# Kernel optimization log

Measured on AMD Instinct MI355X. Metric: run time of the kernel, lower is better.

Reference implementation:

```python
import jax, jax.numpy as jnp
import numpy as np

B, S, D_MODEL, H = 4, 2048, 1024, 16
HD = D_MODEL // H  # head dim = 64


def setup_inputs() -> dict:
    key = jax.random.key(0)
    k1, k2, k3, k4 = jax.random.split(key, 4)
    x = jax.random.normal(k1, (B, S, D_MODEL), dtype=jnp.float32)
    # weights stored as [d_in, d_out] so projection is x @ W
    scale = 1.0 / np.sqrt(D_MODEL)
    Wq = jax.random.normal(k2, (D_MODEL, D_MODEL), dtype=jnp.float32) * scale
    Wk = jax.random.normal(k3, (D_MODEL, D_MODEL), dtype=jnp.float32) * scale
    Wv = jax.random.normal(k4, (D_MODEL, D_MODEL), dtype=jnp.float32) * scale
    return {"x": x, "Wq": Wq, "Wk": Wk, "Wv": Wv}


def reference(x, Wq, Wk, Wv):
    b, s, d_in = x.shape
    h, hd = H, HD
    # project and split heads -> [b, h, s, hd]
    q = (x @ Wq).reshape(b, s, h, hd).transpose(0, 2, 1, 3)
    k = (x @ Wk).reshape(b, s, h, hd).transpose(0, 2, 1, 3)
    v = (x @ Wv).reshape(b, s, h, hd).transpose(0, 2, 1, 3)
    # raw scores [b, h, s, s]; causal mask (strict upper triangle -> -inf)
    scores = jnp.einsum("bhqd,bhkd->bhqk", q, k)
    causal = jnp.tril(jnp.ones((s, s), dtype=bool))
    scores = jnp.where(causal, scores, -jnp.inf)
    attn = jax.nn.softmax(scores / jnp.sqrt(jnp.float32(hd)), axis=-1)
    ctx = jnp.einsum("bhqk,bhkd->bhqd", attn, v)
    return ctx.transpose(0, 2, 1, 3).reshape(b, s, h * hd)
```

## Files before the change

kernel.cpp:

```cpp
#include <hip/hip_runtime.h>

typedef unsigned short u16;
typedef unsigned int u32;
typedef __bf16 bf16_t;
typedef bf16_t bf16x8 __attribute__((ext_vector_type(8)));
typedef bf16_t bf16x4_t __attribute__((ext_vector_type(4)));
typedef float f32x4 __attribute__((ext_vector_type(4)));

#define S_LEN 2048
#define DM 1024
#define NH 16
#define HDIM 64
#define PSTR 80

__device__ __forceinline__ u16 f2b(float f) {
  u32 u = __builtin_bit_cast(u32, f);
  u32 r = (u + 0x7FFFu + ((u >> 16) & 1u)) >> 16;
  return (u16)r;
}

__device__ __forceinline__ void gload16(const void* g, void* l) {
  __builtin_amdgcn_global_load_lds((const __attribute__((address_space(1))) void*)g,
                                   (__attribute__((address_space(3))) void*)l,
                                   16, 0, 0);
}

__device__ __forceinline__ bf16x8 ld_bf8(const u16* p) {
  return *reinterpret_cast<const bf16x8*>(p);
}

__device__ __forceinline__ void stage_tile(const u16* __restrict__ base, int stride,
                                           u16* __restrict__ dst, int tid) {
#pragma unroll
  for (int i = 0; i < 2; ++i) {
    int ci = i * 256 + tid;
    int row = ci >> 3, col = ci & 7;
    gload16(base + (size_t)row * stride + ((col ^ (row & 7)) << 3), dst + ci * 8);
  }
}

__device__ __forceinline__ bf16x8 ld_swz(const u16* lds, int row, int chunk) {
  return ld_bf8(lds + row * 64 + ((chunk ^ (row & 7)) << 3));
}

__global__ __launch_bounds__(256) void k_cvt(const float* __restrict__ in, u16* __restrict__ out) {
  int i = (blockIdx.x * 256 + threadIdx.x) * 4;
  float4 v = *reinterpret_cast<const float4*>(in + i);
  ushort4 o = make_ushort4(f2b(v.x), f2b(v.y), f2b(v.z), f2b(v.w));
  *reinterpret_cast<ushort4*>(out + i) = o;
}

__global__ __launch_bounds__(256) void k_wt(const float* __restrict__ W, u16* __restrict__ Wt) {
  __shared__ float t[32][33];
  int n0 = blockIdx.x * 32, k0 = blockIdx.y * 32;
  int tx = threadIdx.x & 31, ty = threadIdx.x >> 5;
#pragma unroll
  for (int i = 0; i < 32; i += 8)
    t[ty + i][tx] = W[(size_t)(k0 + ty + i) * DM + n0 + tx];
  __syncthreads();
#pragma unroll
  for (int i = 0; i < 32; i += 8)
    Wt[(size_t)(n0 + ty + i) * DM + k0 + tx] = f2b(t[tx][ty + i]);
}

__global__ __launch_bounds__(256) void k_gemm(const u16* __restrict__ Xb, const u16* __restrict__ Wt_all,
                                              u16* __restrict__ Out_all, float qscale) {
  __shared__ u16 At[128 * 32];
  __shared__ u16 Bt[128 * 32];
  int j = blockIdx.x;
  int sw = (j & 7) * 192 + (j >> 3);
  int bx = sw % 24, by = sw / 24;
  int tid = threadIdx.x;
  int lane = tid & 63, w = tid >> 6;
  int l15 = lane & 15, lg = lane >> 4;
  int wm = w >> 1, wn = w & 1;
  int n0g = bx * 128, m0 = by * 128;
  int which = n0g >> 10;
  int n0 = n0g & 1023;
  float scale = (which == 0) ? qscale : 1.0f;
  u16* Out = Out_all + (size_t)which * (size_t)(4 * NH * S_LEN * HDIM);
  f32x4 acc[4][4] = {};
  for (int kt = 0; kt < DM / 32; ++kt) {
    int kk = kt * 32;
#pragma unroll
    for (int i = 0; i < 2; ++i) {
      int t2 = i * 256 + tid;
      int row = t2 >> 2, c16 = t2 & 3;
      gload16(Xb + (size_t)(m0 + row) * DM + kk + c16 * 8, At + t2 * 8);
      gload16(Wt_all + (size_t)(n0g + row) * DM + kk + c16 * 8, Bt + t2 * 8);
    }
    __syncthreads();
    bf16x8 af[4], bfr[4];
#pragma unroll
    for (int mi = 0; mi < 4; ++mi)
      af[mi] = ld_bf8(At + (wm * 64 + mi * 16 + l15) * 32 + lg * 8);
#pragma unroll
    for (int ni = 0; ni < 4; ++ni)
      bfr[ni] = ld_bf8(Bt + (wn * 64 + ni * 16 + l15) * 32 + lg * 8);
#pragma unroll
    for (int mi = 0; mi < 4; ++mi)
#pragma unroll
      for (int ni = 0; ni < 4; ++ni)
        acc[mi][ni] = __builtin_amdgcn_mfma_f32_16x16x32_bf16(af[mi], bfr[ni], acc[mi][ni], 0, 0, 0);
    __syncthreads();
  }
#pragma unroll
  for (int mi = 0; mi < 4; ++mi) {
#pragma unroll
    for (int ni = 0; ni < 4; ++ni) {
#pragma unroll
      for (int r = 0; r < 4; ++r) {
        int m = m0 + wm * 64 + mi * 16 + lg * 4 + r;
        int n = n0 + wn * 64 + ni * 16 + l15;
        int b = m >> 11, s = m & 2047;
        int h = n >> 6, hd = n & 63;
        Out[(((size_t)(b * NH + h)) * S_LEN + s) * HDIM + hd] = f2b(acc[mi][ni][r] * scale);
      }
    }
  }
}

__global__ __launch_bounds__(256) void k_vt(const u16* __restrict__ V, u16* __restrict__ Vt) {
  __shared__ u16 t[32][33];
  int hd0 = blockIdx.x * 32, s0 = blockIdx.y * 32;
  size_t base = (size_t)blockIdx.z * S_LEN * HDIM;
  int tx = threadIdx.x & 31, ty = threadIdx.x >> 5;
#pragma unroll
  for (int i = 0; i < 32; i += 8)
    t[ty + i][tx] = V[base + (size_t)(s0 + ty + i) * HDIM + hd0 + tx];
  __syncthreads();
#pragma unroll
  for (int i = 0; i < 32; i += 8)
    Vt[base + (size_t)(hd0 + ty + i) * S_LEN + s0 + tx] = t[tx][ty + i];
}

__device__ __forceinline__ void attn_strip(const u16* __restrict__ Qp, const u16* __restrict__ Kp,
                                           const u16* __restrict__ Vp, float* __restrict__ out,
                                           int b, int h, int qbase, int w, int tid, int lane, int nt,
                                           u16 (*Kd)[64 * 64], u16* __restrict__ Vd,
                                           u16* __restrict__ Pw) {
  int l15 = lane & 15, lg = lane >> 4;
  int qrow = qbase + w * 16;
  bf16x8 qf0 = ld_bf8(Qp + (size_t)(qrow + l15) * HDIM + lg * 8);
  bf16x8 qf1 = ld_bf8(Qp + (size_t)(qrow + l15) * HDIM + 32 + lg * 8);
  f32x4 o[4] = {};
  float ls = 0.f;
  int qa = qrow + l15;

  stage_tile(Kp, HDIM, Kd[0], tid);
  asm volatile("s_waitcnt vmcnt(0)" ::: "memory");
  __builtin_amdgcn_sched_barrier(0);
  __builtin_amdgcn_s_barrier();
  __builtin_amdgcn_sched_barrier(0);

  for (int kt = 0; kt < nt; ++kt) {
    int k0 = kt * 64;
    int cur = kt & 1;
    bool pre = (kt + 1 < nt);
    stage_tile(Vp + k0, S_LEN, Vd, tid);
    if (pre) stage_tile(Kp + (size_t)(k0 + 64) * HDIM, HDIM, Kd[cur ^ 1], tid);

    f32x4 sc[4];
    __builtin_amdgcn_s_setprio(1);
#pragma unroll
    for (int kb = 0; kb < 4; ++kb) {
      bf16x8 kf0 = ld_swz(Kd[cur], kb * 16 + l15, lg);
      bf16x8 kf1 = ld_swz(Kd[cur], kb * 16 + l15, 4 + lg);
      f32x4 z = {};
      z = __builtin_amdgcn_mfma_f32_16x16x32_bf16(kf0, qf0, z, 0, 0, 0);
      sc[kb] = __builtin_amdgcn_mfma_f32_16x16x32_bf16(kf1, qf1, sc[kb] = z, 0, 0, 0);
    }
    __builtin_amdgcn_s_setprio(0);

    if (kt == nt - 1) {
#pragma unroll
      for (int kb = 0; kb < 4; ++kb) {
        bf16x4_t pw;
#pragma unroll
        for (int r = 0; r < 4; ++r) {
          int key = k0 + kb * 16 + lg * 4 + r;
          float e = __builtin_amdgcn_exp2f(sc[kb][r]);
          e = (key > qa) ? 0.f : e;
          ls += e;
          pw[r] = (bf16_t)e;
        }
        *reinterpret_cast<bf16x4_t*>(Pw + l15 * PSTR + kb * 16 + lg * 4) = pw;
      }
    } else {
#pragma unroll
      for (int kb = 0; kb < 4; ++kb) {
        bf16x4_t pw;
#pragma unroll
        for (int r = 0; r < 4; ++r) {
          float e = __builtin_amdgcn_exp2f(sc[kb][r]);
          ls += e;
          pw[r] = (bf16_t)e;
        }
        *reinterpret_cast<bf16x4_t*>(Pw + l15 * PSTR + kb * 16 + lg * 4) = pw;
      }
    }
    asm volatile("" ::: "memory");
    bf16x8 pf0 = ld_bf8(Pw + l15 * PSTR + lg * 8);
    bf16x8 pf1 = ld_bf8(Pw + l15 * PSTR + 32 + lg * 8);

    if (pre) asm volatile("s_waitcnt vmcnt(2) lgkmcnt(0)" ::: "memory");
    else     asm volatile("s_waitcnt vmcnt(0) lgkmcnt(0)" ::: "memory");
    __builtin_amdgcn_sched_barrier(0);
    __builtin_amdgcn_s_barrier();
    __builtin_amdgcn_sched_barrier(0);

    __builtin_amdgcn_s_setprio(1);
#pragma unroll
    for (int n = 0; n < 4; ++n) {
      bf16x8 vf0 = ld_swz(Vd, n * 16 + l15, lg);
      bf16x8 vf1 = ld_swz(Vd, n * 16 + l15, 4 + lg);
      o[n] = __builtin_amdgcn_mfma_f32_16x16x32_bf16(pf0, vf0, o[n], 0, 0, 0);
      o[n] = __builtin_amdgcn_mfma_f32_16x16x32_bf16(pf1, vf1, o[n], 0, 0, 0);
    }
    __builtin_amdgcn_s_setprio(0);

    asm volatile("s_waitcnt vmcnt(0) lgkmcnt(0)" ::: "memory");
    __builtin_amdgcn_sched_barrier(0);
    __builtin_amdgcn_s_barrier();
    __builtin_amdgcn_sched_barrier(0);
  }

  ls += __shfl_xor(ls, 16);
  ls += __shfl_xor(ls, 32);
  float l0 = __shfl(ls, lg * 4 + 0);
  float l1 = __shfl(ls, lg * 4 + 1);
  float l2 = __shfl(ls, lg * 4 + 2);
  float l3 = __shfl(ls, lg * 4 + 3);
  float lsr[4] = {l0, l1, l2, l3};
#pragma unroll
  for (int r = 0; r < 4; ++r) {
    float inv = 1.f / lsr[r];
    int row = qrow + lg * 4 + r;
#pragma unroll
    for (int n = 0; n < 4; ++n)
      out[((size_t)b * S_LEN + row) * DM + h * HDIM + n * 16 + l15] = o[n][r] * inv;
  }
}

__global__ __launch_bounds__(256, 4) void k_attn(const u16* __restrict__ Qb, const u16* __restrict__ Kb,
                                                 const u16* __restrict__ Vtb, float* __restrict__ out) {
  __shared__ u16 Kd[2][64 * 64];
  __shared__ u16 Vd[64 * 64];
  __shared__ u16 Plds[4][16 * PSTR];
  int j = blockIdx.x;
  int m = j >> 3;
  int x = m & 15;
  int bh = (j & 7) + 8 * (m >> 4);
  int tid = threadIdx.x, lane = tid & 63, w = tid >> 6;
  int b = bh >> 4, h = bh & 15;
  const u16* Qp = Qb + (size_t)bh * S_LEN * HDIM;
  const u16* Kp = Kb + (size_t)bh * S_LEN * HDIM;
  const u16* Vp = Vtb + (size_t)bh * HDIM * S_LEN;
  u16* Pw = Plds[w];
  attn_strip(Qp, Kp, Vp, out, b, h, x * 64, w, tid, lane, x + 1, Kd, Vd, Pw);
  attn_strip(Qp, Kp, Vp, out, b, h, (31 - x) * 64, w, tid, lane, 32 - x, Kd, Vd, Pw);
}

extern "C" void kernel_launch(void* const* d_in, const int* in_sizes, int n_in,
                              void* d_out, int out_size, void* d_ws, size_t ws_size,
                              hipStream_t stream) {
  const float* x  = (const float*)d_in[0];
  const float* Wq = (const float*)d_in[1];
  const float* Wk = (const float*)d_in[2];
  const float* Wv = (const float*)d_in[3];
  float* out = (float*)d_out;

  u16* ws  = (u16*)d_ws;
  u16* xb  = ws;
  u16* wqt = xb + 8388608;
  u16* wkt = wqt + 1048576;
  u16* wvt = wkt + 1048576;
  u16* Qb  = wvt + 1048576;
  u16* Kb  = Qb + 8388608;
  u16* Vb  = Kb + 8388608;
  u16* Vtb = Vb + 8388608;

  const float qscale = 0.125f * 1.44269504088896f;

  k_cvt<<<8192, 256, 0, stream>>>(x, xb);
  k_wt<<<dim3(32, 32), 256, 0, stream>>>(Wq, wqt);
  k_wt<<<dim3(32, 32), 256, 0, stream>>>(Wk, wkt);
  k_wt<<<dim3(32, 32), 256, 0, stream>>>(Wv, wvt);
  k_gemm<<<1536, 256, 0, stream>>>(xb, wqt, Qb, qscale);
  k_vt<<<dim3(2, 64, 64), 256, 0, stream>>>(Vb, Vtb);
  k_attn<<<1024, 256, 0, stream>>>(Qb, Kb, Vtb, out);
}
```

Before: 150.2 us.

## Restructure QKV GEMM into double-buffered 256x192 tiles with swizzled LDS

The fused QKV projection GEMM moves from 128x128 tiles with single-buffered K=32 steps to 256x192 tiles, 512 threads, and K=64 steps. LDS is double-buffered with XOR-swizzled layout, and next-tile global->LDS loads are interleaved between MFMA phases. This aims to raise arithmetic intensity per loaded byte, cut barrier and sync overhead per FLOP, and avoid LDS bank conflicts. In exchange it uses more LDS (about 112 KB per block) and more registers, and a 192-wide tile can now straddle the Q/K/V boundary, so the output target is chosen per column.

```diff
diff --git a/kernel.cpp b/kernel.cpp
--- a/kernel.cpp
+++ b/kernel.cpp
@@ -29,8 +29,15 @@
   return *reinterpret_cast<const bf16x8*>(p);
 }
 
-__device__ __forceinline__ void stage_tile(const u16* __restrict__ base, int stride,
-                                           u16* __restrict__ dst, int tid) {
+__device__ __forceinline__ void stage_chunk(const u16* __restrict__ g, int stride,
+                                            u16* __restrict__ dst, int tid) {
+  int srow = tid >> 3;
+  int scol = ((tid & 7) ^ (srow & 7)) << 3;
+  gload16(g + (size_t)srow * stride + scol, dst + tid * 8);
+}
+
+__device__ __forceinline__ void stage_tile256(const u16* __restrict__ base, int stride,
+                                              u16* __restrict__ dst, int tid) {
 #pragma unroll
   for (int i = 0; i < 2; ++i) {
     int ci = i * 256 + tid;
@@ -39,7 +46,7 @@
   }
 }
 
-__device__ __forceinline__ bf16x8 ld_swz(const u16* lds, int row, int chunk) {
+__device__ __forceinline__ bf16x8 ld_swz64(const u16* lds, int row, int chunk) {
   return ld_bf8(lds + row * 64 + ((chunk ^ (row & 7)) << 3));
 }
 
@@ -63,61 +70,102 @@
     Wt[(size_t)(n0 + ty + i) * DM + k0 + tx] = f2b(t[tx][ty + i]);
 }
 
-__global__ __launch_bounds__(256) void k_gemm(const u16* __restrict__ Xb, const u16* __restrict__ Wt_all,
-                                              u16* __restrict__ Out_all, float qscale) {
-  __shared__ u16 At[128 * 32];
-  __shared__ u16 Bt[128 * 32];
+__global__ __launch_bounds__(512, 2) void k_gemm(const u16* __restrict__ Xb, const u16* __restrict__ Wt_all,
+                                                 u16* __restrict__ Out_all, float qscale) {
+  __shared__ __attribute__((aligned(16))) u16 Asb[2][256 * 64];
+  __shared__ __attribute__((aligned(16))) u16 Bsb[2][192 * 64];
   int j = blockIdx.x;
-  int sw = (j & 7) * 192 + (j >> 3);
-  int bx = sw % 24, by = sw / 24;
+  int sw = (j & 7) * 64 + (j >> 3);
+  int bx = sw & 15, by = sw >> 4;
+  int n0g = bx * 192, m0 = by * 256;
   int tid = threadIdx.x;
   int lane = tid & 63, w = tid >> 6;
   int l15 = lane & 15, lg = lane >> 4;
-  int wm = w >> 1, wn = w & 1;
-  int n0g = bx * 128, m0 = by * 128;
-  int which = n0g >> 10;
-  int n0 = n0g & 1023;
-  float scale = (which == 0) ? qscale : 1.0f;
-  u16* Out = Out_all + (size_t)which * (size_t)(4 * NH * S_LEN * HDIM);
-  f32x4 acc[4][4] = {};
-  for (int kt = 0; kt < DM / 32; ++kt) {
-    int kk = kt * 32;
-#pragma unroll
-    for (int i = 0; i < 2; ++i) {
-      int t2 = i * 256 + tid;
-      int row = t2 >> 2, c16 = t2 & 3;
-      gload16(Xb + (size_t)(m0 + row) * DM + kk + c16 * 8, At + t2 * 8);
-      gload16(Wt_all + (size_t)(n0g + row) * DM + kk + c16 * 8, Bt + t2 * 8);
-    }
-    __syncthreads();
-    bf16x8 af[4], bfr[4];
-#pragma unroll
-    for (int mi = 0; mi < 4; ++mi)
-      af[mi] = ld_bf8(At + (wm * 64 + mi * 16 + l15) * 32 + lg * 8);
-#pragma unroll
-    for (int ni = 0; ni < 4; ++ni)
-      bfr[ni] = ld_bf8(Bt + (wn * 64 + ni * 16 + l15) * 32 + lg * 8);
-#pragma unroll
-    for (int mi = 0; mi < 4; ++mi)
-#pragma unroll
-      for (int ni = 0; ni < 4; ++ni)
-        acc[mi][ni] = __builtin_amdgcn_mfma_f32_16x16x32_bf16(af[mi], bfr[ni], acc[mi][ni], 0, 0, 0);
-    __syncthreads();
-  }
-#pragma unroll
-  for (int mi = 0; mi < 4; ++mi) {
-#pragma unroll
-    for (int ni = 0; ni < 4; ++ni) {
+  int wm = w >> 2, wn = w & 3;
+
+  const u16* Ag = Xb + (size_t)m0 * DM;
+  const u16* Bg = Wt_all + (size_t)n0g * DM;
+
+#define STAGE_A(c, kt, buf) stage_chunk(Ag + (size_t)((c) * 64) * DM + (kt) * 64, DM, Asb[buf] + (c) * 4096, tid)
+#define STAGE_B(c, kt, buf) stage_chunk(Bg + (size_t)((c) * 64) * DM + (kt) * 64, DM, Bsb[buf] + (c) * 4096, tid)
+
+  f32x4 acc[8][3] = {};
+  bf16x8 bfr[3][2];
+
+  STAGE_A(0, 0, 0); STAGE_A(1, 0, 0); STAGE_A(2, 0, 0); STAGE_A(3, 0, 0);
+  STAGE_B(0, 0, 0); STAGE_B(1, 0, 0); STAGE_B(2, 0, 0);
+  __syncthreads();
+
+  for (int t = 0; t < 16; ++t) {
+    int cur = t & 1, nxt = cur ^ 1;
+    bool pre = (t + 1 < 16);
+    const u16* Ab = Asb[cur];
+    const u16* Bb = Bsb[cur];
+#pragma unroll
+    for (int p = 0; p < 4; ++p) {
+      bf16x8 af[2][2];
+#pragma unroll
+      for (int m2 = 0; m2 < 2; ++m2)
+#pragma unroll
+        for (int ks = 0; ks < 2; ++ks)
+          af[m2][ks] = ld_swz64(Ab, wm * 128 + (2 * p + m2) * 16 + l15, ks * 4 + lg);
+      if (p == 0) {
+#pragma unroll
+        for (int ni = 0; ni < 3; ++ni)
+#pragma unroll
+          for (int ks = 0; ks < 2; ++ks)
+            bfr[ni][ks] = ld_swz64(Bb, wn * 48 + ni * 16 + l15, ks * 4 + lg);
+      }
+      if (pre) {
+        if (p == 0)      { STAGE_A(0, t + 1, nxt); STAGE_A(1, t + 1, nxt); STAGE_B(0, t + 1, nxt); }
+        else if (p == 1) { STAGE_A(2, t + 1, nxt); STAGE_A(3, t + 1, nxt); STAGE_B(1, t + 1, nxt); }
+        else if (p == 2) { STAGE_B(2, t + 1, nxt); }
+      }
+      __builtin_amdgcn_sched_barrier(0);
+      __builtin_amdgcn_s_barrier();
+      __builtin_amdgcn_sched_barrier(0);
+      __builtin_amdgcn_s_setprio(1);
+#pragma unroll
+      for (int m2 = 0; m2 < 2; ++m2)
+#pragma unroll
+        for (int ni = 0; ni < 3; ++ni)
+#pragma unroll
+          for (int ks = 0; ks < 2; ++ks)
+            acc[2 * p + m2][ni] =
+                __builtin_amdgcn_mfma_f32_16x16x32_bf16(af[m2][ks], bfr[ni][ks], acc[2 * p + m2][ni], 0, 0, 0);
+      __builtin_amdgcn_s_setprio(0);
+      __builtin_amdgcn_sched_barrier(0);
+      if (p < 3) {
+        __builtin_amdgcn_s_barrier();
+        __builtin_amdgcn_sched_barrier(0);
+      }
+    }
+    asm volatile("s_waitcnt vmcnt(0)" ::: "memory");
+    __builtin_amdgcn_sched_barrier(0);
+    __builtin_amdgcn_s_barrier();
+    __builtin_amdgcn_sched_barrier(0);
+  }
+
+#pragma unroll
+  for (int mi = 0; mi < 8; ++mi) {
+#pragma unroll
+    for (int ni = 0; ni < 3; ++ni) {
+      int n = n0g + wn * 48 + ni * 16 + l15;
+      int which = n >> 10;
+      int nn = n & 1023;
+      int h = nn >> 6, hd = nn & 63;
+      float scale = (which == 0) ? qscale : 1.0f;
+      u16* Out = Out_all + (size_t)which * (size_t)(4 * NH * S_LEN * HDIM);
 #pragma unroll
       for (int r = 0; r < 4; ++r) {
-        int m = m0 + wm * 64 + mi * 16 + lg * 4 + r;
-        int n = n0 + wn * 64 + ni * 16 + l15;
+        int m = m0 + wm * 128 + mi * 16 + lg * 4 + r;
         int b = m >> 11, s = m & 2047;
-        int h = n >> 6, hd = n & 63;
         Out[(((size_t)(b * NH + h)) * S_LEN + s) * HDIM + hd] = f2b(acc[mi][ni][r] * scale);
       }
     }
   }
+#undef STAGE_A
+#undef STAGE_B
 }
 
 __global__ __launch_bounds__(256) void k_vt(const u16* __restrict__ V, u16* __restrict__ Vt) {
@@ -147,7 +195,7 @@
   float ls = 0.f;
   int qa = qrow + l15;
 
-  stage_tile(Kp, HDIM, Kd[0], tid);
+  stage_tile256(Kp, HDIM, Kd[0], tid);
   asm volatile("s_waitcnt vmcnt(0)" ::: "memory");
   __builtin_amdgcn_sched_barrier(0);
   __builtin_amdgcn_s_barrier();
@@ -157,15 +205,15 @@
     int k0 = kt * 64;
     int cur = kt & 1;
     bool pre = (kt + 1 < nt);
-    stage_tile(Vp + k0, S_LEN, Vd, tid);
-    if (pre) stage_tile(Kp + (size_t)(k0 + 64) * HDIM, HDIM, Kd[cur ^ 1], tid);
+    stage_tile256(Vp + k0, S_LEN, Vd, tid);
+    if (pre) stage_tile256(Kp + (size_t)(k0 + 64) * HDIM, HDIM, Kd[cur ^ 1], tid);
 
     f32x4 sc[4];
     __builtin_amdgcn_s_setprio(1);
 #pragma unroll
     for (int kb = 0; kb < 4; ++kb) {
-      bf16x8 kf0 = ld_swz(Kd[cur], kb * 16 + l15, lg);
-      bf16x8 kf1 = ld_swz(Kd[cur], kb * 16 + l15, 4 + lg);
+      bf16x8 kf0 = ld_swz64(Kd[cur], kb * 16 + l15, lg);
+      bf16x8 kf1 = ld_swz64(Kd[cur], kb * 16 + l15, 4 + lg);
       f32x4 z = {};
       z = __builtin_amdgcn_mfma_f32_16x16x32_bf16(kf0, qf0, z, 0, 0, 0);
       sc[kb] = __builtin_amdgcn_mfma_f32_16x16x32_bf16(kf1, qf1, sc[kb] = z, 0, 0, 0);
@@ -212,8 +260,8 @@
     __builtin_amdgcn_s_setprio(1);
 #pragma unroll
     for (int n = 0; n < 4; ++n) {
-      bf16x8 vf0 = ld_swz(Vd, n * 16 + l15, lg);
-      bf16x8 vf1 = ld_swz(Vd, n * 16 + l15, 4 + lg);
+      bf16x8 vf0 = ld_swz64(Vd, n * 16 + l15, lg);
+      bf16x8 vf1 = ld_swz64(Vd, n * 16 + l15, 4 + lg);
       o[n] = __builtin_amdgcn_mfma_f32_16x16x32_bf16(pf0, vf0, o[n], 0, 0, 0);
       o[n] = __builtin_amdgcn_mfma_f32_16x16x32_bf16(pf1, vf1, o[n], 0, 0, 0);
     }
@@ -286,7 +334,7 @@
   k_wt<<<dim3(32, 32), 256, 0, stream>>>(Wq, wqt);
   k_wt<<<dim3(32, 32), 256, 0, stream>>>(Wk, wkt);
   k_wt<<<dim3(32, 32), 256, 0, stream>>>(Wv, wvt);
-  k_gemm<<<1536, 256, 0, stream>>>(xb, wqt, Qb, qscale);
+  k_gemm<<<512, 512, 0, stream>>>(xb, wqt, Qb, qscale);
   k_vt<<<dim3(2, 64, 64), 256, 0, stream>>>(Vb, Vtb);
   k_attn<<<1024, 256, 0, stream>>>(Qb, Kb, Vtb, out);
 }
```

New measurement: 145.3 us. 1.03x faster.

## Fuse V transpose into projection GEMM epilogue and swizzle GEMM LDS tiles

Applied to the files above, without the earlier changes.

The V-projection blocks of the GEMM now transpose their output tile through shared memory and write V^T directly, which removes the separate k_vt kernel and the intermediate V buffer round trip. The GEMM shared-memory A/B tiles use an XOR swizzle to cut LDS bank conflicts on fragment loads. The attention loop gains an explicit barrier with a partial vmcnt wait before the QK step and drops the trailing full vmcnt wait, changing how K/V prefetch overlaps with compute. The risks are a larger shared allocation in the GEMM, which may reduce occupancy, and the reworked wait counts, which must stay correct.

```diff
diff --git a/kernel.cpp b/kernel.cpp
--- a/kernel.cpp
+++ b/kernel.cpp
@@ -6,12 +6,14 @@
 typedef bf16_t bf16x8 __attribute__((ext_vector_type(8)));
 typedef bf16_t bf16x4_t __attribute__((ext_vector_type(4)));
 typedef float f32x4 __attribute__((ext_vector_type(4)));
+typedef unsigned short ushort8_t __attribute__((ext_vector_type(8)));
 
 #define S_LEN 2048
 #define DM 1024
 #define NH 16
 #define HDIM 64
 #define PSTR 80
+#define TSTR 136
 
 __device__ __forceinline__ u16 f2b(float f) {
   u32 u = __builtin_bit_cast(u32, f);
@@ -29,8 +31,8 @@
   return *reinterpret_cast<const bf16x8*>(p);
 }
 
-__device__ __forceinline__ void stage_tile(const u16* __restrict__ base, int stride,
-                                           u16* __restrict__ dst, int tid) {
+__device__ __forceinline__ void stage_tile256(const u16* __restrict__ base, int stride,
+                                              u16* __restrict__ dst, int tid) {
 #pragma unroll
   for (int i = 0; i < 2; ++i) {
     int ci = i * 256 + tid;
@@ -38,9 +40,21 @@
     gload16(base + (size_t)row * stride + ((col ^ (row & 7)) << 3), dst + ci * 8);
   }
 }
-
-__device__ __forceinline__ bf16x8 ld_swz(const u16* lds, int row, int chunk) {
+__device__ __forceinline__ bf16x8 ld_swz64(const u16* lds, int row, int chunk) {
   return ld_bf8(lds + row * 64 + ((chunk ^ (row & 7)) << 3));
+}
+
+__device__ __forceinline__ void stage_tile32(const u16* __restrict__ base,
+                                             u16* __restrict__ dst, int tid) {
+#pragma unroll
+  for (int i = 0; i < 2; ++i) {
+    int ci = i * 256 + tid;
+    int row = ci >> 2, ch = ci & 3;
+    gload16(base + (size_t)row * DM + ((ch ^ ((row >> 1) & 3)) << 3), dst + ci * 8);
+  }
+}
+__device__ __forceinline__ bf16x8 ld_swz32(const u16* lds, int row, int chunk) {
+  return ld_bf8(lds + row * 32 + ((chunk ^ ((row >> 1) & 3)) << 3));
 }
 
 __global__ __launch_bounds__(256) void k_cvt(const float* __restrict__ in, u16* __restrict__ out) {
@@ -64,39 +78,38 @@
 }
 
 __global__ __launch_bounds__(256) void k_gemm(const u16* __restrict__ Xb, const u16* __restrict__ Wt_all,
-                                              u16* __restrict__ Out_all, float qscale) {
-  __shared__ u16 At[128 * 32];
-  __shared__ u16 Bt[128 * 32];
+                                              u16* __restrict__ Out_all, u16* __restrict__ Vt,
+                                              float qscale) {
+  __shared__ __attribute__((aligned(16))) u16 smem[128 * TSTR];
+  u16* At = smem;
+  u16* Bt = smem + 4096;
   int j = blockIdx.x;
   int sw = (j & 7) * 192 + (j >> 3);
   int bx = sw % 24, by = sw / 24;
+  int n0g = bx * 128, m0 = by * 128;
+  int which = n0g >> 10;
+  int n0 = n0g & 1023;
   int tid = threadIdx.x;
   int lane = tid & 63, w = tid >> 6;
   int l15 = lane & 15, lg = lane >> 4;
   int wm = w >> 1, wn = w & 1;
-  int n0g = bx * 128, m0 = by * 128;
-  int which = n0g >> 10;
-  int n0 = n0g & 1023;
-  float scale = (which == 0) ? qscale : 1.0f;
-  u16* Out = Out_all + (size_t)which * (size_t)(4 * NH * S_LEN * HDIM);
+
+  const u16* Ag = Xb + (size_t)m0 * DM;
+  const u16* Bg = Wt_all + (size_t)n0g * DM;
+
   f32x4 acc[4][4] = {};
-  for (int kt = 0; kt < DM / 32; ++kt) {
+  for (int kt = 0; kt < 32; ++kt) {
     int kk = kt * 32;
-#pragma unroll
-    for (int i = 0; i < 2; ++i) {
-      int t2 = i * 256 + tid;
-      int row = t2 >> 2, c16 = t2 & 3;
-      gload16(Xb + (size_t)(m0 + row) * DM + kk + c16 * 8, At + t2 * 8);
-      gload16(Wt_all + (size_t)(n0g + row) * DM + kk + c16 * 8, Bt + t2 * 8);
-    }
+    stage_tile32(Ag + kk, At, tid);
+    stage_tile32(Bg + kk, Bt, tid);
     __syncthreads();
     bf16x8 af[4], bfr[4];
 #pragma unroll
     for (int mi = 0; mi < 4; ++mi)
-      af[mi] = ld_bf8(At + (wm * 64 + mi * 16 + l15) * 32 + lg * 8);
+      af[mi] = ld_swz32(At, wm * 64 + mi * 16 + l15, lg);
 #pragma unroll
     for (int ni = 0; ni < 4; ++ni)
-      bfr[ni] = ld_bf8(Bt + (wn * 64 + ni * 16 + l15) * 32 + lg * 8);
+      bfr[ni] = ld_swz32(Bt, wn * 64 + ni * 16 + l15, lg);
 #pragma unroll
     for (int mi = 0; mi < 4; ++mi)
 #pragma unroll
@@ -104,34 +117,48 @@
         acc[mi][ni] = __builtin_amdgcn_mfma_f32_16x16x32_bf16(af[mi], bfr[ni], acc[mi][ni], 0, 0, 0);
     __syncthreads();
   }
-#pragma unroll
-  for (int mi = 0; mi < 4; ++mi) {
-#pragma unroll
-    for (int ni = 0; ni < 4; ++ni) {
-#pragma unroll
-      for (int r = 0; r < 4; ++r) {
-        int m = m0 + wm * 64 + mi * 16 + lg * 4 + r;
-        int n = n0 + wn * 64 + ni * 16 + l15;
-        int b = m >> 11, s = m & 2047;
-        int h = n >> 6, hd = n & 63;
-        Out[(((size_t)(b * NH + h)) * S_LEN + s) * HDIM + hd] = f2b(acc[mi][ni][r] * scale);
+
+  if (which < 2) {
+    float scale = (which == 0) ? qscale : 1.0f;
+    u16* Out = Out_all + (size_t)which * (size_t)(4 * NH * S_LEN * HDIM);
+#pragma unroll
+    for (int mi = 0; mi < 4; ++mi) {
+#pragma unroll
+      for (int ni = 0; ni < 4; ++ni) {
+#pragma unroll
+        for (int r = 0; r < 4; ++r) {
+          int m = m0 + wm * 64 + mi * 16 + lg * 4 + r;
+          int n = n0 + wn * 64 + ni * 16 + l15;
+          int b = m >> 11, s = m & 2047;
+          int h = n >> 6, hd = n & 63;
+          Out[(((size_t)(b * NH + h)) * S_LEN + s) * HDIM + hd] = f2b(acc[mi][ni][r] * scale);
+        }
       }
     }
-  }
-}
-
-__global__ __launch_bounds__(256) void k_vt(const u16* __restrict__ V, u16* __restrict__ Vt) {
-  __shared__ u16 t[32][33];
-  int hd0 = blockIdx.x * 32, s0 = blockIdx.y * 32;
-  size_t base = (size_t)blockIdx.z * S_LEN * HDIM;
-  int tx = threadIdx.x & 31, ty = threadIdx.x >> 5;
-#pragma unroll
-  for (int i = 0; i < 32; i += 8)
-    t[ty + i][tx] = V[base + (size_t)(s0 + ty + i) * HDIM + hd0 + tx];
-  __syncthreads();
-#pragma unroll
-  for (int i = 0; i < 32; i += 8)
-    Vt[base + (size_t)(hd0 + ty + i) * S_LEN + s0 + tx] = t[tx][ty + i];
+  } else {
+    u16* T = smem;
+#pragma unroll
+    for (int mi = 0; mi < 4; ++mi) {
+#pragma unroll
+      for (int ni = 0; ni < 4; ++ni) {
+        ushort4 w4 = make_ushort4(f2b(acc[mi][ni][0]), f2b(acc[mi][ni][1]),
+                                  f2b(acc[mi][ni][2]), f2b(acc[mi][ni][3]));
+        *reinterpret_cast<ushort4*>(T + (wn * 64 + ni * 16 + l15) * TSTR +
+                                    wm * 64 + mi * 16 + lg * 4) = w4;
+      }
+    }
+    __syncthreads();
+    int base_h = n0 >> 6;
+    int b = m0 >> 11, s0 = m0 & 2047;
+#pragma unroll
+    for (int pass = 0; pass < 8; ++pass) {
+      int row = pass * 16 + (tid >> 4);
+      int col = (tid & 15) * 8;
+      ushort8_t v = *reinterpret_cast<const ushort8_t*>(T + row * TSTR + col);
+      int h = base_h + (row >> 6), hd = row & 63;
+      *reinterpret_cast<ushort8_t*>(Vt + ((size_t)((b * NH + h) * HDIM + hd)) * S_LEN + s0 + col) = v;
+    }
+  }
 }
 
 __device__ __forceinline__ void attn_strip(const u16* __restrict__ Qp, const u16* __restrict__ Kp,
@@ -147,7 +174,7 @@
   float ls = 0.f;
   int qa = qrow + l15;
 
-  stage_tile(Kp, HDIM, Kd[0], tid);
+  stage_tile256(Kp, HDIM, Kd[0], tid);
   asm volatile("s_waitcnt vmcnt(0)" ::: "memory");
   __builtin_amdgcn_sched_barrier(0);
   __builtin_amdgcn_s_barrier();
@@ -157,15 +184,21 @@
     int k0 = kt * 64;
     int cur = kt & 1;
     bool pre = (kt + 1 < nt);
-    stage_tile(Vp + k0, S_LEN, Vd, tid);
-    if (pre) stage_tile(Kp + (size_t)(k0 + 64) * HDIM, HDIM, Kd[cur ^ 1], tid);
+    stage_tile256(Vp + k0, S_LEN, Vd, tid);
+    if (pre) stage_tile256(Kp + (size_t)(k0 + 64) * HDIM, HDIM, Kd[cur ^ 1], tid);
+
+    if (pre) asm volatile("s_waitcnt vmcnt(4)" ::: "memory");
+    else     asm volatile("s_waitcnt vmcnt(2)" ::: "memory");
+    __builtin_amdgcn_sched_barrier(0);
+    __builtin_amdgcn_s_barrier();
+    __builtin_amdgcn_sched_barrier(0);
 
     f32x4 sc[4];
     __builtin_amdgcn_s_setprio(1);
 #pragma unroll
     for (int kb = 0; kb < 4; ++kb) {
-      bf16x8 kf0 = ld_swz(Kd[cur], kb * 16 + l15, lg);
-      bf16x8 kf1 = ld_swz(Kd[cur], kb * 16 + l15, 4 + lg);
+      bf16x8 kf0 = ld_swz64(Kd[cur], kb * 16 + l15, lg);
+      bf16x8 kf1 = ld_swz64(Kd[cur], kb * 16 + l15, 4 + lg);
       f32x4 z = {};
       z = __builtin_amdgcn_mfma_f32_16x16x32_bf16(kf0, qf0, z, 0, 0, 0);
       sc[kb] = __builtin_amdgcn_mfma_f32_16x16x32_bf16(kf1, qf1, sc[kb] = z, 0, 0, 0);
@@ -212,14 +245,13 @@
     __builtin_amdgcn_s_setprio(1);
 #pragma unroll
     for (int n = 0; n < 4; ++n) {
-      bf16x8 vf0 = ld_swz(Vd, n * 16 + l15, lg);
-      bf16x8 vf1 = ld_swz(Vd, n * 16 + l15, 4 + lg);
+      bf16x8 vf0 = ld_swz64(Vd, n * 16 + l15, lg);
+      bf16x8 vf1 = ld_swz64(Vd, n * 16 + l15, 4 + lg);
       o[n] = __builtin_amdgcn_mfma_f32_16x16x32_bf16(pf0, vf0, o[n], 0, 0, 0);
       o[n] = __builtin_amdgcn_mfma_f32_16x16x32_bf16(pf1, vf1, o[n], 0, 0, 0);
     }
     __builtin_amdgcn_s_setprio(0);
 
-    asm volatile("s_waitcnt vmcnt(0) lgkmcnt(0)" ::: "memory");
     __builtin_amdgcn_sched_barrier(0);
     __builtin_amdgcn_s_barrier();
     __builtin_amdgcn_sched_barrier(0);
@@ -277,8 +309,7 @@
   u16* wvt = wkt + 1048576;
   u16* Qb  = wvt + 1048576;
   u16* Kb  = Qb + 8388608;
-  u16* Vb  = Kb + 8388608;
-  u16* Vtb = Vb + 8388608;
+  u16* Vtb = Kb + 8388608;
 
   const float qscale = 0.125f * 1.44269504088896f;
 
@@ -286,7 +317,6 @@
   k_wt<<<dim3(32, 32), 256, 0, stream>>>(Wq, wqt);
   k_wt<<<dim3(32, 32), 256, 0, stream>>>(Wk, wkt);
   k_wt<<<dim3(32, 32), 256, 0, stream>>>(Wv, wvt);
-  k_gemm<<<1536, 256, 0, stream>>>(xb, wqt, Qb, qscale);
-  k_vt<<<dim3(2, 64, 64), 256, 0, stream>>>(Vb, Vtb);
+  k_gemm<<<1536, 256, 0, stream>>>(xb, wqt, Qb, Vtb, qscale);
   k_attn<<<1024, 256, 0, stream>>>(Qb, Kb, Vtb, out);
 }
```

Measured after the change: 145.5 us. 1.03x faster.
